# Optimization experiments

Measured on AMD Instinct MI355X. Metric: run time of the kernel, lower is better.

The kernel has to match this reference:

```python
import jax, jax.numpy as jnp
import numpy as np

B, S, H, NH = 8, 1024, 1024, 16
HD = H // NH  # 64


def setup_inputs() -> dict:
    key = jax.random.key(0)
    ks = jax.random.split(key, 7)
    scale = 1.0 / np.sqrt(H)
    return {
        "hidden_states": jax.random.normal(ks[0], (B, S, H), jnp.float32),
        "Wq": jax.random.normal(ks[1], (H, H), jnp.float32) * scale,
        "bq": jax.random.normal(ks[2], (H,), jnp.float32) * 0.01,
        "Wk": jax.random.normal(ks[3], (H, H), jnp.float32) * scale,
        "bk": jax.random.normal(ks[4], (H,), jnp.float32) * 0.01,
        "Wv": jax.random.normal(ks[5], (H, H), jnp.float32) * scale,
        "bv": jax.random.normal(ks[6], (H,), jnp.float32) * 0.01,
    }


def _split_heads(x):
    # [B, S, H] -> [B, NH, S, HD]
    b, s, _ = x.shape
    return x.reshape(b, s, NH, HD).transpose(0, 2, 1, 3)


def reference(hidden_states, Wq, bq, Wk, bk, Wv, bv):
    q = _split_heads(hidden_states @ Wq.T + bq)
    k = _split_heads(hidden_states @ Wk.T + bk)
    v = _split_heads(hidden_states @ Wv.T + bv)
    scale = 1.0 / np.sqrt(HD).astype(np.float32)
    # [B, NH, S, S] attention logits (module materializes this fully)
    scores = jnp.einsum('bhld,bhsd->bhls', q, k) * scale
    probs = jax.nn.softmax(scores, axis=-1)  # dropout_p=0.0 -> no dropout
    ctx = jnp.einsum('bhls,bhsd->bhld', probs, v)
    # [B, NH, S, HD] -> [B, S, H]
    ctx = ctx.transpose(0, 2, 1, 3).reshape(hidden_states.shape[0], hidden_states.shape[1], H)
    return ctx
```

## Files before the change

kernel.cpp:

```cpp
#include <hip/hip_runtime.h>
#include <hip/hip_bf16.h>
#include <stdint.h>

#define B_  8
#define S_  1024
#define H_  1024
#define NH_ 16
#define HD_ 64
#define M_  (B_*S_)

using bf16x8 = __attribute__((ext_vector_type(8))) __bf16;
using f32x4  = __attribute__((ext_vector_type(4))) float;
using f32x16 = __attribute__((ext_vector_type(16))) float;
typedef int iv2 __attribute__((ext_vector_type(2)));

#define LOG2E 1.4426950408889634f

#if __has_builtin(__builtin_amdgcn_exp2f)
#define EXP2(x) __builtin_amdgcn_exp2f(x)
#else
#define EXP2(x) exp2f(x)
#endif

#define SBAR() asm volatile("s_barrier" ::: "memory")
#define WAITV(n) asm volatile("s_waitcnt vmcnt(" #n ")" ::: "memory")

__device__ __forceinline__ void gload_lds16(const void* g, void* l) {
  __builtin_amdgcn_global_load_lds(
      (const __attribute__((address_space(1))) unsigned int*)g,
      (__attribute__((address_space(3))) unsigned int*)l, 16, 0, 0);
}

__device__ __forceinline__ unsigned pack_bf16(float lo, float hi) {
  unsigned r;
  asm("v_cvt_pk_bf16_f32 %0, %1, %2" : "=v"(r) : "v"(lo), "v"(hi));
  return r;
}

__device__ __forceinline__ void swapl32(unsigned& a, unsigned& b) {
#if __has_builtin(__builtin_amdgcn_permlane32_swap)
  iv2 r = __builtin_amdgcn_permlane32_swap((int)a, (int)b, false, false);
  a = (unsigned)r[0];
  b = (unsigned)r[1];
#else
  unsigned axc = (unsigned)__shfl_xor((int)a, 32);
  unsigned bxc = (unsigned)__shfl_xor((int)b, 32);
  int lane = threadIdx.x & 63;
  unsigned an = (lane < 32) ? a : bxc;
  unsigned bn = (lane < 32) ? axc : b;
  a = an; b = bn;
#endif
}

__global__ void __launch_bounds__(256) cast_bf16_kernel(const float* __restrict__ in,
                                                        __bf16* __restrict__ out, int n8) {
  int i = blockIdx.x * blockDim.x + threadIdx.x;
  int stride = gridDim.x * blockDim.x;
  for (; i < n8; i += stride) {
    float4 f0 = ((const float4*)in)[2 * i];
    float4 f1 = ((const float4*)in)[2 * i + 1];
    bf16x8 o;
    o[0] = (__bf16)f0.x; o[1] = (__bf16)f0.y; o[2] = (__bf16)f0.z; o[3] = (__bf16)f0.w;
    o[4] = (__bf16)f1.x; o[5] = (__bf16)f1.y; o[6] = (__bf16)f1.z; o[7] = (__bf16)f1.w;
    ((bf16x8*)out)[i] = o;
  }
}

__global__ void __launch_bounds__(256) cast3_bf16_kernel(
    const float* __restrict__ s0, const float* __restrict__ s1,
    const float* __restrict__ s2, __bf16* __restrict__ dst) {
  int i = blockIdx.x * blockDim.x + threadIdx.x;
  int seg = i >> 17, rem = i & 131071;
  const float* s = (seg == 0) ? s0 : ((seg == 1) ? s1 : s2);
  float4 f0 = ((const float4*)s)[2 * rem];
  float4 f1 = ((const float4*)s)[2 * rem + 1];
  bf16x8 o;
  o[0] = (__bf16)f0.x; o[1] = (__bf16)f0.y; o[2] = (__bf16)f0.z; o[3] = (__bf16)f0.w;
  o[4] = (__bf16)f1.x; o[5] = (__bf16)f1.y; o[6] = (__bf16)f1.z; o[7] = (__bf16)f1.w;
  ((bf16x8*)dst)[i] = o;
}

__global__ void __launch_bounds__(256) qkv_gemm_kernel(
    const __bf16* __restrict__ X,
    const __bf16* __restrict__ Wq, const __bf16* __restrict__ Wk, const __bf16* __restrict__ Wv,
    const float* __restrict__ bq, const float* __restrict__ bk, const float* __restrict__ bv,
    __bf16* __restrict__ Qo, __bf16* __restrict__ Ko, __bf16* __restrict__ Vto) {
  __shared__ __align__(16) char Asm[128 * 128];
  __shared__ __align__(16) char Bsm[128 * 128];

  const int tid = threadIdx.x;
  const int lane = tid & 63, w = tid >> 6;
  const int l15 = lane & 15, g = lane >> 4;
  const int wr = w >> 1, wc = w & 1;
  const int m0 = blockIdx.x * 128;
  const int n0 = blockIdx.y * 128;
  const int z = blockIdx.z;
  const __bf16* W = (z == 0) ? Wq : ((z == 1) ? Wk : Wv);
  const float* bias = (z == 0) ? bq : ((z == 1) ? bk : bv);

  f32x4 acc[4][4] = {};

  for (int kt = 0; kt < H_; kt += 64) {
    __syncthreads();
#pragma unroll
    for (int is = 0; is < 4; ++is) {
      int q = is * 4096 + tid * 16;
      int row = q >> 7;
      int inrow = (q & 127) ^ ((row & 7) << 4);
      const char* ga = (const char*)X + (size_t)(m0 + row) * (H_ * 2) + kt * 2 + inrow;
      const char* gb = (const char*)W + (size_t)(n0 + row) * (H_ * 2) + kt * 2 + inrow;
      gload_lds16(ga, Asm + is * 4096 + w * 1024);
      gload_lds16(gb, Bsm + is * 4096 + w * 1024);
    }
    __syncthreads();
#pragma unroll
    for (int ks = 0; ks < 2; ++ks) {
      bf16x8 a[4], b[4];
#pragma unroll
      for (int i = 0; i < 4; ++i) {
        int row = wr * 64 + i * 16 + l15;
        int chunk = (g + ks * 4) ^ (row & 7);
        a[i] = *reinterpret_cast<const bf16x8*>(Asm + row * 128 + chunk * 16);
      }
#pragma unroll
      for (int j = 0; j < 4; ++j) {
        int row = wc * 64 + j * 16 + l15;
        int chunk = (g + ks * 4) ^ (row & 7);
        b[j] = *reinterpret_cast<const bf16x8*>(Bsm + row * 128 + chunk * 16);
      }
#pragma unroll
      for (int i = 0; i < 4; ++i)
#pragma unroll
        for (int j = 0; j < 4; ++j)
          acc[i][j] = __builtin_amdgcn_mfma_f32_16x16x32_bf16(a[i], b[j], acc[i][j], 0, 0, 0);
    }
  }

#pragma unroll
  for (int i = 0; i < 4; ++i) {
#pragma unroll
    for (int j = 0; j < 4; ++j) {
      int n = n0 + wc * 64 + j * 16 + l15;
      float bs = bias[n];
      int nh = n >> 6, d = n & 63;
#pragma unroll
      for (int r = 0; r < 4; ++r) {
        int m = m0 + wr * 64 + i * 16 + 4 * g + r;
        int bb = m >> 10, s = m & 1023;
        float v = acc[i][j][r] + bs;
        if (z == 0) {
          Qo[(((size_t)bb * NH_ + nh) * S_ + s) * HD_ + d] = (__bf16)(v * (0.125f * LOG2E));
        } else if (z == 1) {
          Ko[(((size_t)bb * NH_ + nh) * S_ + s) * HD_ + d] = (__bf16)v;
        } else {
          Vto[(((size_t)bb * NH_ + nh) * HD_ + d) * S_ + s] = (__bf16)v;
        }
      }
    }
  }
}

#define CROW(r, hi) (((r) & 3) + 8 * ((r) >> 2) + 4 * (hi))

__global__ void __launch_bounds__(512) attn_kernel(
    const __bf16* __restrict__ Q,
    const __bf16* __restrict__ K,
    const __bf16* __restrict__ Vt,
    float* __restrict__ Out) {
  __shared__ __align__(16) char Ksm[2][8192];
  __shared__ __align__(16) char Vsm[2][8192];
  __shared__ __align__(16) float stat_lds[512];

  const int tid = threadIdx.x, lane = tid & 63, w = tid >> 6;
  const int l31 = lane & 31, hi = lane >> 5;
  const int head = blockIdx.y;
  const int bb = head >> 4, nh = head & 15;
  const int qw = blockIdx.x * 256 + w * 32;

  const char* Qh = (const char*)(Q + (size_t)head * S_ * HD_);
  const char* Kh = (const char*)(K + (size_t)head * S_ * HD_);
  const char* Vh = (const char*)(Vt + (size_t)head * S_ * HD_);

  const int srow = (tid * 16) >> 7;
  const int sinrow = ((tid * 16) & 127) ^ ((srow & 7) << 4);

  bf16x8 qf[4];
#pragma unroll
  for (int slot = 0; slot < 4; ++slot)
    qf[slot] = *reinterpret_cast<const bf16x8*>(
        Qh + (size_t)(qw + l31) * 128 + slot * 32 + hi * 16);

  float m_run = -1e30f, l_run = 0.0f;
  f32x16 accO[2] = {};

  gload_lds16(Kh + (size_t)srow * 128 + sinrow, Ksm[0] + w * 1024);
  gload_lds16(Vh + (size_t)srow * 2048 + sinrow, Vsm[0] + w * 1024);

  for (int t = 0; t < 16; ++t) {
    const int cur = t & 1;
    if (t < 15) {
      const int nxt = cur ^ 1;
      const size_t kvn = (size_t)(t + 1) * 64;
      gload_lds16(Kh + (size_t)(kvn + srow) * 128 + sinrow, Ksm[nxt] + w * 1024);
      gload_lds16(Vh + (size_t)srow * 2048 + kvn * 2 + sinrow, Vsm[nxt] + w * 1024);
      WAITV(2);
    } else {
      WAITV(0);
    }
    SBAR();

    const char* Kc = Ksm[cur];
    const char* Vc = Vsm[cur];

    f32x16 s0 = {}, s1 = {};
    __builtin_amdgcn_s_setprio(1);
#pragma unroll
    for (int slot = 0; slot < 4; ++slot) {
      int c0 = slot * 2 + hi;
      int r0 = l31;
      bf16x8 k0 = *reinterpret_cast<const bf16x8*>(Kc + r0 * 128 + ((c0 ^ (r0 & 7)) << 4));
      int r1 = 32 + l31;
      bf16x8 k1 = *reinterpret_cast<const bf16x8*>(Kc + r1 * 128 + ((c0 ^ (r1 & 7)) << 4));
      s0 = __builtin_amdgcn_mfma_f32_32x32x16_bf16(k0, qf[slot], s0, 0, 0, 0);
      s1 = __builtin_amdgcn_mfma_f32_32x32x16_bf16(k1, qf[slot], s1, 0, 0, 0);
    }
    __builtin_amdgcn_s_setprio(0);

    float mx = -1e30f;
#pragma unroll
    for (int r = 0; r < 16; ++r) mx = fmaxf(mx, fmaxf(s0[r], s1[r]));
    mx = fmaxf(mx, __shfl_xor(mx, 32));
    float mnew = fmaxf(m_run, mx);
    float corr = EXP2(m_run - mnew);
    float sum = 0.0f;
#pragma unroll
    for (int r = 0; r < 16; ++r) {
      float p0 = EXP2(s0[r] - mnew); s0[r] = p0; sum += p0;
      float p1 = EXP2(s1[r] - mnew); s1[r] = p1; sum += p1;
    }
    sum += __shfl_xor(sum, 32);
    l_run = l_run * corr + sum;
    m_run = mnew;

    stat_lds[w * 64 + lane] = corr;
    f32x4 c4[4];
#pragma unroll
    for (int rq = 0; rq < 4; ++rq)
      c4[rq] = *reinterpret_cast<const f32x4*>(&stat_lds[w * 64 + rq * 8 + hi * 4]);
#pragma unroll
    for (int r = 0; r < 16; ++r) {
      float cr = c4[r >> 2][r & 3];
      accO[0][r] *= cr;
      accO[1][r] *= cr;
    }

    bf16x8 pa[4];
#define BUILD_PA(T, rb)                                                     \
    {                                                                       \
      unsigned x1 = pack_bf16(T[rb + 0], T[rb + 1]);                        \
      unsigned x2 = pack_bf16(T[rb + 2], T[rb + 3]);                        \
      unsigned y1 = pack_bf16(T[rb + 4], T[rb + 5]);                        \
      unsigned y2 = pack_bf16(T[rb + 6], T[rb + 7]);                        \
      swapl32(x1, y1);                                                      \
      swapl32(x2, y2);                                                      \
      union { unsigned u[4]; bf16x8 v; } cvt;                               \
      cvt.u[0] = x1; cvt.u[1] = x2; cvt.u[2] = y1; cvt.u[3] = y2;           \
      pa_out = cvt.v;                                                       \
    }
    {
      bf16x8 pa_out;
      BUILD_PA(s0, 0) pa[0] = pa_out;
      BUILD_PA(s0, 8) pa[1] = pa_out;
      BUILD_PA(s1, 0) pa[2] = pa_out;
      BUILD_PA(s1, 8) pa[3] = pa_out;
    }

    __builtin_amdgcn_s_setprio(1);
#pragma unroll
    for (int ks = 0; ks < 4; ++ks) {
#pragma unroll
      for (int dt = 0; dt < 2; ++dt) {
        int rd = dt * 32 + l31;
        int ck = ks * 2 + hi;
        bf16x8 vb = *reinterpret_cast<const bf16x8*>(Vc + rd * 128 + ((ck ^ (rd & 7)) << 4));
        accO[dt] = __builtin_amdgcn_mfma_f32_32x32x16_bf16(pa[ks], vb, accO[dt], 0, 0, 0);
      }
    }
    __builtin_amdgcn_s_setprio(0);

    SBAR();
  }

  stat_lds[w * 64 + lane] = 1.0f / l_run;
  f32x4 li4[4];
#pragma unroll
  for (int rq = 0; rq < 4; ++rq)
    li4[rq] = *reinterpret_cast<const f32x4*>(&stat_lds[w * 64 + rq * 8 + hi * 4]);

  float* Ob = Out + (size_t)bb * S_ * H_ + (size_t)nh * HD_;
#pragma unroll
  for (int r = 0; r < 16; ++r) {
    int qabs = qw + CROW(r, hi);
    float li = li4[r >> 2][r & 3];
#pragma unroll
    for (int dt = 0; dt < 2; ++dt) {
      int d = dt * 32 + l31;
      Ob[(size_t)qabs * H_ + d] = accO[dt][r] * li;
    }
  }
}

extern "C" void kernel_launch(void* const* d_in, const int* in_sizes, int n_in,
                              void* d_out, int out_size, void* d_ws, size_t ws_size,
                              hipStream_t stream) {
  const float* hs = (const float*)d_in[0];
  const float* Wq = (const float*)d_in[1];
  const float* bq = (const float*)d_in[2];
  const float* Wk = (const float*)d_in[3];
  const float* bk = (const float*)d_in[4];
  const float* Wv = (const float*)d_in[5];
  const float* bv = (const float*)d_in[6];
  float* out = (float*)d_out;
  char* ws = (char*)d_ws;

  size_t off = 0;
  __bf16* Xb  = (__bf16*)(ws + off); off += (size_t)M_ * H_ * 2;
  __bf16* Wqb = (__bf16*)(ws + off); off += (size_t)H_ * H_ * 2;
  __bf16* Wkb = (__bf16*)(ws + off); off += (size_t)H_ * H_ * 2;
  __bf16* Wvb = (__bf16*)(ws + off); off += (size_t)H_ * H_ * 2;
  __bf16* Qb  = (__bf16*)(ws + off); off += (size_t)M_ * H_ * 2;
  __bf16* Kb  = (__bf16*)(ws + off); off += (size_t)M_ * H_ * 2;
  __bf16* Vtb = (__bf16*)(ws + off); off += (size_t)M_ * H_ * 2;

  cast_bf16_kernel<<<4096, 256, 0, stream>>>(hs, Xb, M_ * H_ / 8);
  cast3_bf16_kernel<<<1536, 256, 0, stream>>>(Wq, Wk, Wv, Wqb);

  qkv_gemm_kernel<<<dim3(M_ / 128, H_ / 128, 3), 256, 0, stream>>>(
      Xb, Wqb, Wkb, Wvb, bq, bk, bv, Qb, Kb, Vtb);

  attn_kernel<<<dim3(S_ / 256, B_ * NH_), 512, 0, stream>>>(Qb, Kb, Vtb, out);
}
```

Before: 150.6 us.

## Rewrite QKV GEMM with 256x192 tiles, double-buffered LDS pipeline, fused weight matrix

The QKV projection GEMM now treats the three weight matrices as one concatenated 3072-wide matrix and uses 512-thread blocks computing 256x192 tiles. K-tile loads go into double-buffered dynamic LDS (112 KB) and are interleaved with the MFMA phases, using s_setprio and partial vmcnt waits. A swizzled block index is added for L2 locality. The goal is to hide global load latency and raise MFMA utilization over the single-buffered 128x128 version, at the cost of heavy LDS use that limits occupancy and a more fragile synchronization scheme.

```diff
diff --git a/kernel.cpp b/kernel.cpp
--- a/kernel.cpp
+++ b/kernel.cpp
@@ -80,80 +80,178 @@
   ((bf16x8*)dst)[i] = o;
 }
 
-__global__ void __launch_bounds__(256) qkv_gemm_kernel(
-    const __bf16* __restrict__ X,
-    const __bf16* __restrict__ Wq, const __bf16* __restrict__ Wk, const __bf16* __restrict__ Wv,
+#define LDSA(s) (lds + (size_t)(s) * 32768)
+#define LDSB(s) (lds + 65536 + (size_t)(s) * 24576)
+
+__global__ void __launch_bounds__(512, 2) qkv_gemm_kernel(
+    const __bf16* __restrict__ X, const __bf16* __restrict__ Wcat,
     const float* __restrict__ bq, const float* __restrict__ bk, const float* __restrict__ bv,
     __bf16* __restrict__ Qo, __bf16* __restrict__ Ko, __bf16* __restrict__ Vto) {
-  __shared__ __align__(16) char Asm[128 * 128];
-  __shared__ __align__(16) char Bsm[128 * 128];
+  extern __shared__ char lds[];
 
   const int tid = threadIdx.x;
   const int lane = tid & 63, w = tid >> 6;
   const int l15 = lane & 15, g = lane >> 4;
-  const int wr = w >> 1, wc = w & 1;
-  const int m0 = blockIdx.x * 128;
-  const int n0 = blockIdx.y * 128;
-  const int z = blockIdx.z;
-  const __bf16* W = (z == 0) ? Wq : ((z == 1) ? Wk : Wv);
-  const float* bias = (z == 0) ? bq : ((z == 1) ? bk : bv);
-
-  f32x4 acc[4][4] = {};
-
-  for (int kt = 0; kt < H_; kt += 64) {
-    __syncthreads();
-#pragma unroll
-    for (int is = 0; is < 4; ++is) {
-      int q = is * 4096 + tid * 16;
-      int row = q >> 7;
-      int inrow = (q & 127) ^ ((row & 7) << 4);
-      const char* ga = (const char*)X + (size_t)(m0 + row) * (H_ * 2) + kt * 2 + inrow;
-      const char* gb = (const char*)W + (size_t)(n0 + row) * (H_ * 2) + kt * 2 + inrow;
-      gload_lds16(ga, Asm + is * 4096 + w * 1024);
-      gload_lds16(gb, Bsm + is * 4096 + w * 1024);
-    }
-    __syncthreads();
-#pragma unroll
-    for (int ks = 0; ks < 2; ++ks) {
-      bf16x8 a[4], b[4];
-#pragma unroll
-      for (int i = 0; i < 4; ++i) {
-        int row = wr * 64 + i * 16 + l15;
-        int chunk = (g + ks * 4) ^ (row & 7);
-        a[i] = *reinterpret_cast<const bf16x8*>(Asm + row * 128 + chunk * 16);
-      }
-#pragma unroll
-      for (int j = 0; j < 4; ++j) {
-        int row = wc * 64 + j * 16 + l15;
-        int chunk = (g + ks * 4) ^ (row & 7);
-        b[j] = *reinterpret_cast<const bf16x8*>(Bsm + row * 128 + chunk * 16);
-      }
-#pragma unroll
-      for (int i = 0; i < 4; ++i)
-#pragma unroll
-        for (int j = 0; j < 4; ++j)
-          acc[i][j] = __builtin_amdgcn_mfma_f32_16x16x32_bf16(a[i], b[j], acc[i][j], 0, 0, 0);
+  const int wm = w >> 2, wn = w & 3;
+
+  const int bid = blockIdx.x;
+  const int swz = ((bid & 7) << 6) | (bid >> 3);
+  const int tm = swz >> 4, tn = swz & 15;
+  const int bm0 = tm * 256, n0 = tn * 192;
+
+  const char* Xb = (const char*)X;
+  const char* Wb = (const char*)Wcat;
+
+  const int row_b = tid >> 3, scB = ((tid & 7) ^ (row_b & 7));
+  const int row_a = tid >> 2, scA = ((tid & 3) ^ ((row_a >> 1) & 3));
+  const char* srcB = Wb + (size_t)(n0 + row_b) * 2048 + scB * 16;
+  const char* srcA = Xb + (size_t)(bm0 + row_a) * 2048 + scA * 16;
+
+#define STG_B(ss, r, ktb) gload_lds16(srcB + (size_t)(r) * 131072 + (ktb), \
+                                      LDSB(ss) + (r) * 8192 + w * 1024)
+#define STG_A(ss, h, rb, ktb) gload_lds16(srcA + (size_t)(rb) * 262144 + (h) * 64 + (ktb), \
+                                          LDSA(ss) + (h) * 16384 + (rb) * 8192 + w * 1024)
+
+  const int aoff = (wm * 128 + l15) * 64 + ((g ^ ((l15 >> 1) & 3)) << 4);
+  const int boffs = (wn * 48 + l15) * 128;
+  const int bsw = l15 & 7;
+
+  f32x4 acc[8][3] = {};
+
+  STG_B(0, 0, 0); STG_B(0, 1, 0); STG_B(0, 2, 0);
+  STG_A(0, 0, 0, 0); STG_A(0, 0, 1, 0);
+  STG_A(0, 1, 0, 0); STG_A(0, 1, 1, 0);
+
+#pragma unroll 2
+  for (int t = 0; t < 16; ++t) {
+    const int s = t & 1, ns = s ^ 1;
+    const bool st = t < 15;
+    const size_t ktb = (size_t)(t + 1) * 128;
+    const char* As = LDSA(s);
+    const char* Bs = LDSB(s);
+
+    WAITV(2);
+    SBAR();
+    bf16x8 b0 = *(const bf16x8*)(Bs + boffs + 0 * 2048 + ((g ^ bsw) << 4));
+    bf16x8 b1 = *(const bf16x8*)(Bs + boffs + 1 * 2048 + ((g ^ bsw) << 4));
+    bf16x8 b2 = *(const bf16x8*)(Bs + boffs + 2 * 2048 + ((g ^ bsw) << 4));
+    {
+      bf16x8 a0 = *(const bf16x8*)(As + aoff + 0 * 1024);
+      bf16x8 a1 = *(const bf16x8*)(As + aoff + 1 * 1024);
+      bf16x8 a2 = *(const bf16x8*)(As + aoff + 2 * 1024);
+      bf16x8 a3 = *(const bf16x8*)(As + aoff + 3 * 1024);
+      if (st) { STG_B(ns, 0, ktb); STG_B(ns, 1, ktb); }
+      __builtin_amdgcn_s_setprio(1);
+      acc[0][0] = __builtin_amdgcn_mfma_f32_16x16x32_bf16(a0, b0, acc[0][0], 0, 0, 0);
+      acc[0][1] = __builtin_amdgcn_mfma_f32_16x16x32_bf16(a0, b1, acc[0][1], 0, 0, 0);
+      acc[0][2] = __builtin_amdgcn_mfma_f32_16x16x32_bf16(a0, b2, acc[0][2], 0, 0, 0);
+      acc[1][0] = __builtin_amdgcn_mfma_f32_16x16x32_bf16(a1, b0, acc[1][0], 0, 0, 0);
+      acc[1][1] = __builtin_amdgcn_mfma_f32_16x16x32_bf16(a1, b1, acc[1][1], 0, 0, 0);
+      acc[1][2] = __builtin_amdgcn_mfma_f32_16x16x32_bf16(a1, b2, acc[1][2], 0, 0, 0);
+      acc[2][0] = __builtin_amdgcn_mfma_f32_16x16x32_bf16(a2, b0, acc[2][0], 0, 0, 0);
+      acc[2][1] = __builtin_amdgcn_mfma_f32_16x16x32_bf16(a2, b1, acc[2][1], 0, 0, 0);
+      acc[2][2] = __builtin_amdgcn_mfma_f32_16x16x32_bf16(a2, b2, acc[2][2], 0, 0, 0);
+      acc[3][0] = __builtin_amdgcn_mfma_f32_16x16x32_bf16(a3, b0, acc[3][0], 0, 0, 0);
+      acc[3][1] = __builtin_amdgcn_mfma_f32_16x16x32_bf16(a3, b1, acc[3][1], 0, 0, 0);
+      acc[3][2] = __builtin_amdgcn_mfma_f32_16x16x32_bf16(a3, b2, acc[3][2], 0, 0, 0);
+      __builtin_amdgcn_s_setprio(0);
+    }
+
+    SBAR();
+    {
+      bf16x8 a4 = *(const bf16x8*)(As + aoff + 4 * 1024);
+      bf16x8 a5 = *(const bf16x8*)(As + aoff + 5 * 1024);
+      bf16x8 a6 = *(const bf16x8*)(As + aoff + 6 * 1024);
+      bf16x8 a7 = *(const bf16x8*)(As + aoff + 7 * 1024);
+      if (st) { STG_B(ns, 2, ktb); STG_A(ns, 0, 0, ktb); }
+      __builtin_amdgcn_s_setprio(1);
+      acc[4][0] = __builtin_amdgcn_mfma_f32_16x16x32_bf16(a4, b0, acc[4][0], 0, 0, 0);
+      acc[4][1] = __builtin_amdgcn_mfma_f32_16x16x32_bf16(a4, b1, acc[4][1], 0, 0, 0);
+      acc[4][2] = __builtin_amdgcn_mfma_f32_16x16x32_bf16(a4, b2, acc[4][2], 0, 0, 0);
+      acc[5][0] = __builtin_amdgcn_mfma_f32_16x16x32_bf16(a5, b0, acc[5][0], 0, 0, 0);
+      acc[5][1] = __builtin_amdgcn_mfma_f32_16x16x32_bf16(a5, b1, acc[5][1], 0, 0, 0);
+      acc[5][2] = __builtin_amdgcn_mfma_f32_16x16x32_bf16(a5, b2, acc[5][2], 0, 0, 0);
+      acc[6][0] = __builtin_amdgcn_mfma_f32_16x16x32_bf16(a6, b0, acc[6][0], 0, 0, 0);
+      acc[6][1] = __builtin_amdgcn_mfma_f32_16x16x32_bf16(a6, b1, acc[6][1], 0, 0, 0);
+      acc[6][2] = __builtin_amdgcn_mfma_f32_16x16x32_bf16(a6, b2, acc[6][2], 0, 0, 0);
+      acc[7][0] = __builtin_amdgcn_mfma_f32_16x16x32_bf16(a7, b0, acc[7][0], 0, 0, 0);
+      acc[7][1] = __builtin_amdgcn_mfma_f32_16x16x32_bf16(a7, b1, acc[7][1], 0, 0, 0);
+      acc[7][2] = __builtin_amdgcn_mfma_f32_16x16x32_bf16(a7, b2, acc[7][2], 0, 0, 0);
+      __builtin_amdgcn_s_setprio(0);
+    }
+
+    if (st) { WAITV(4); } else { WAITV(0); }
+    SBAR();
+    b0 = *(const bf16x8*)(Bs + boffs + 0 * 2048 + (((g + 4) ^ bsw) << 4));
+    b1 = *(const bf16x8*)(Bs + boffs + 1 * 2048 + (((g + 4) ^ bsw) << 4));
+    b2 = *(const bf16x8*)(Bs + boffs + 2 * 2048 + (((g + 4) ^ bsw) << 4));
+    {
+      bf16x8 a0 = *(const bf16x8*)(As + 16384 + aoff + 0 * 1024);
+      bf16x8 a1 = *(const bf16x8*)(As + 16384 + aoff + 1 * 1024);
+      bf16x8 a2 = *(const bf16x8*)(As + 16384 + aoff + 2 * 1024);
+      bf16x8 a3 = *(const bf16x8*)(As + 16384 + aoff + 3 * 1024);
+      if (st) { STG_A(ns, 0, 1, ktb); STG_A(ns, 1, 0, ktb); }
+      __builtin_amdgcn_s_setprio(1);
+      acc[0][0] = __builtin_amdgcn_mfma_f32_16x16x32_bf16(a0, b0, acc[0][0], 0, 0, 0);
+      acc[0][1] = __builtin_amdgcn_mfma_f32_16x16x32_bf16(a0, b1, acc[0][1], 0, 0, 0);
+      acc[0][2] = __builtin_amdgcn_mfma_f32_16x16x32_bf16(a0, b2, acc[0][2], 0, 0, 0);
+      acc[1][0] = __builtin_amdgcn_mfma_f32_16x16x32_bf16(a1, b0, acc[1][0], 0, 0, 0);
+      acc[1][1] = __builtin_amdgcn_mfma_f32_16x16x32_bf16(a1, b1, acc[1][1], 0, 0, 0);
+      acc[1][2] = __builtin_amdgcn_mfma_f32_16x16x32_bf16(a1, b2, acc[1][2], 0, 0, 0);
+      acc[2][0] = __builtin_amdgcn_mfma_f32_16x16x32_bf16(a2, b0, acc[2][0], 0, 0, 0);
+      acc[2][1] = __builtin_amdgcn_mfma_f32_16x16x32_bf16(a2, b1, acc[2][1], 0, 0, 0);
+      acc[2][2] = __builtin_amdgcn_mfma_f32_16x16x32_bf16(a2, b2, acc[2][2], 0, 0, 0);
+      acc[3][0] = __builtin_amdgcn_mfma_f32_16x16x32_bf16(a3, b0, acc[3][0], 0, 0, 0);
+      acc[3][1] = __builtin_amdgcn_mfma_f32_16x16x32_bf16(a3, b1, acc[3][1], 0, 0, 0);
+      acc[3][2] = __builtin_amdgcn_mfma_f32_16x16x32_bf16(a3, b2, acc[3][2], 0, 0, 0);
+      __builtin_amdgcn_s_setprio(0);
+    }
+
+    SBAR();
+    {
+      bf16x8 a4 = *(const bf16x8*)(As + 16384 + aoff + 4 * 1024);
+      bf16x8 a5 = *(const bf16x8*)(As + 16384 + aoff + 5 * 1024);
+      bf16x8 a6 = *(const bf16x8*)(As + 16384 + aoff + 6 * 1024);
+      bf16x8 a7 = *(const bf16x8*)(As + 16384 + aoff + 7 * 1024);
+      if (st) { STG_A(ns, 1, 1, ktb); }
+      __builtin_amdgcn_s_setprio(1);
+      acc[4][0] = __builtin_amdgcn_mfma_f32_16x16x32_bf16(a4, b0, acc[4][0], 0, 0, 0);
+      acc[4][1] = __builtin_amdgcn_mfma_f32_16x16x32_bf16(a4, b1, acc[4][1], 0, 0, 0);
+      acc[4][2] = __builtin_amdgcn_mfma_f32_16x16x32_bf16(a4, b2, acc[4][2], 0, 0, 0);
+      acc[5][0] = __builtin_amdgcn_mfma_f32_16x16x32_bf16(a5, b0, acc[5][0], 0, 0, 0);
+      acc[5][1] = __builtin_amdgcn_mfma_f32_16x16x32_bf16(a5, b1, acc[5][1], 0, 0, 0);
+      acc[5][2] = __builtin_amdgcn_mfma_f32_16x16x32_bf16(a5, b2, acc[5][2], 0, 0, 0);
+      acc[6][0] = __builtin_amdgcn_mfma_f32_16x16x32_bf16(a6, b0, acc[6][0], 0, 0, 0);
+      acc[6][1] = __builtin_amdgcn_mfma_f32_16x16x32_bf16(a6, b1, acc[6][1], 0, 0, 0);
+      acc[6][2] = __builtin_amdgcn_mfma_f32_16x16x32_bf16(a6, b2, acc[6][2], 0, 0, 0);
+      acc[7][0] = __builtin_amdgcn_mfma_f32_16x16x32_bf16(a7, b0, acc[7][0], 0, 0, 0);
+      acc[7][1] = __builtin_amdgcn_mfma_f32_16x16x32_bf16(a7, b1, acc[7][1], 0, 0, 0);
+      acc[7][2] = __builtin_amdgcn_mfma_f32_16x16x32_bf16(a7, b2, acc[7][2], 0, 0, 0);
+      __builtin_amdgcn_s_setprio(0);
     }
   }
 
 #pragma unroll
-  for (int i = 0; i < 4; ++i) {
-#pragma unroll
-    for (int j = 0; j < 4; ++j) {
-      int n = n0 + wc * 64 + j * 16 + l15;
-      float bs = bias[n];
-      int nh = n >> 6, d = n & 63;
+  for (int nf = 0; nf < 3; ++nf) {
+    const int ng = n0 + wn * 48 + nf * 16 + l15;
+    const int z = ng >> 10;
+    const int nzn = ng & 1023;
+    const float* bp = (z == 0) ? bq : ((z == 1) ? bk : bv);
+    const float bs = bp[nzn];
+    const int nh = nzn >> 6, d = nzn & 63;
+#pragma unroll
+    for (int mf = 0; mf < 8; ++mf) {
 #pragma unroll
       for (int r = 0; r < 4; ++r) {
-        int m = m0 + wr * 64 + i * 16 + 4 * g + r;
-        int bb = m >> 10, s = m & 1023;
-        float v = acc[i][j][r] + bs;
+        const int m = bm0 + wm * 128 + mf * 16 + 4 * g + r;
+        const int bb = m >> 10, sI = m & 1023;
+        const float v = acc[mf][nf][r] + bs;
         if (z == 0) {
-          Qo[(((size_t)bb * NH_ + nh) * S_ + s) * HD_ + d] = (__bf16)(v * (0.125f * LOG2E));
+          Qo[(((size_t)bb * NH_ + nh) * S_ + sI) * HD_ + d] = (__bf16)(v * (0.125f * LOG2E));
         } else if (z == 1) {
-          Ko[(((size_t)bb * NH_ + nh) * S_ + s) * HD_ + d] = (__bf16)v;
+          Ko[(((size_t)bb * NH_ + nh) * S_ + sI) * HD_ + d] = (__bf16)v;
         } else {
-          Vto[(((size_t)bb * NH_ + nh) * HD_ + d) * S_ + s] = (__bf16)v;
+          Vto[(((size_t)bb * NH_ + nh) * HD_ + d) * S_ + sI] = (__bf16)v;
         }
       }
     }
@@ -331,12 +429,16 @@
   __bf16* Qb  = (__bf16*)(ws + off); off += (size_t)M_ * H_ * 2;
   __bf16* Kb  = (__bf16*)(ws + off); off += (size_t)M_ * H_ * 2;
   __bf16* Vtb = (__bf16*)(ws + off); off += (size_t)M_ * H_ * 2;
+  (void)Wkb; (void)Wvb;
+
+  (void)hipFuncSetAttribute((const void*)qkv_gemm_kernel,
+                            hipFuncAttributeMaxDynamicSharedMemorySize, 114688);
 
   cast_bf16_kernel<<<4096, 256, 0, stream>>>(hs, Xb, M_ * H_ / 8);
   cast3_bf16_kernel<<<1536, 256, 0, stream>>>(Wq, Wk, Wv, Wqb);
 
-  qkv_gemm_kernel<<<dim3(M_ / 128, H_ / 128, 3), 256, 0, stream>>>(
-      Xb, Wqb, Wkb, Wvb, bq, bk, bv, Qb, Kb, Vtb);
+  qkv_gemm_kernel<<<512, 512, 114688, stream>>>(
+      Xb, Wqb, bq, bk, bv, Qb, Kb, Vtb);
 
   attn_kernel<<<dim3(S_ / 256, B_ * NH_), 512, 0, stream>>>(Qb, Kb, Vtb, out);
 }
```

After: 152.8 us. About the same (+1.4%).

## Double-buffer QKV GEMM LDS tiles with K=32 steps and async prefetch

Applied to the files above, without the earlier changes.

The QKV projection GEMM moves from a single 64-wide K tile with two full barriers per step to double-buffered 32-wide K tiles. The next tile is issued with global-to-LDS loads before the MFMAs on the current tile, and partial vmcnt waits are used. The swizzle is changed to suit 64-byte rows, and MFMA sections get raised wave priority. The aim is to hide global load latency behind compute, at the cost of twice as many loop iterations and barriers.

```diff
diff --git a/kernel.cpp b/kernel.cpp
--- a/kernel.cpp
+++ b/kernel.cpp
@@ -85,8 +85,8 @@
     const __bf16* __restrict__ Wq, const __bf16* __restrict__ Wk, const __bf16* __restrict__ Wv,
     const float* __restrict__ bq, const float* __restrict__ bk, const float* __restrict__ bv,
     __bf16* __restrict__ Qo, __bf16* __restrict__ Ko, __bf16* __restrict__ Vto) {
-  __shared__ __align__(16) char Asm[128 * 128];
-  __shared__ __align__(16) char Bsm[128 * 128];
+  __shared__ __align__(16) char Asm[2][8192];
+  __shared__ __align__(16) char Bsm[2][8192];
 
   const int tid = threadIdx.x;
   const int lane = tid & 63, w = tid >> 6;
@@ -98,42 +98,61 @@
   const __bf16* W = (z == 0) ? Wq : ((z == 1) ? Wk : Wv);
   const float* bias = (z == 0) ? bq : ((z == 1) ? bk : bv);
 
+  const int srow0 = tid >> 2;
+  const int schunk0 = (tid & 3) ^ ((srow0 >> 1) & 3);
+  const int srow1 = 64 + srow0;
+  const int schunk1 = (tid & 3) ^ ((srow1 >> 1) & 3);
+  const char* gA0 = (const char*)X + (size_t)(m0 + srow0) * 2048 + schunk0 * 16;
+  const char* gA1 = (const char*)X + (size_t)(m0 + srow1) * 2048 + schunk1 * 16;
+  const char* gB0 = (const char*)W + (size_t)(n0 + srow0) * 2048 + schunk0 * 16;
+  const char* gB1 = (const char*)W + (size_t)(n0 + srow1) * 2048 + schunk1 * 16;
+
   f32x4 acc[4][4] = {};
 
-  for (int kt = 0; kt < H_; kt += 64) {
-    __syncthreads();
-#pragma unroll
-    for (int is = 0; is < 4; ++is) {
-      int q = is * 4096 + tid * 16;
-      int row = q >> 7;
-      int inrow = (q & 127) ^ ((row & 7) << 4);
-      const char* ga = (const char*)X + (size_t)(m0 + row) * (H_ * 2) + kt * 2 + inrow;
-      const char* gb = (const char*)W + (size_t)(n0 + row) * (H_ * 2) + kt * 2 + inrow;
-      gload_lds16(ga, Asm + is * 4096 + w * 1024);
-      gload_lds16(gb, Bsm + is * 4096 + w * 1024);
-    }
-    __syncthreads();
-#pragma unroll
-    for (int ks = 0; ks < 2; ++ks) {
-      bf16x8 a[4], b[4];
-#pragma unroll
-      for (int i = 0; i < 4; ++i) {
-        int row = wr * 64 + i * 16 + l15;
-        int chunk = (g + ks * 4) ^ (row & 7);
-        a[i] = *reinterpret_cast<const bf16x8*>(Asm + row * 128 + chunk * 16);
-      }
-#pragma unroll
-      for (int j = 0; j < 4; ++j) {
-        int row = wc * 64 + j * 16 + l15;
-        int chunk = (g + ks * 4) ^ (row & 7);
-        b[j] = *reinterpret_cast<const bf16x8*>(Bsm + row * 128 + chunk * 16);
-      }
-#pragma unroll
-      for (int i = 0; i < 4; ++i)
-#pragma unroll
-        for (int j = 0; j < 4; ++j)
-          acc[i][j] = __builtin_amdgcn_mfma_f32_16x16x32_bf16(a[i], b[j], acc[i][j], 0, 0, 0);
-    }
+  gload_lds16(gA0, Asm[0] + w * 1024);
+  gload_lds16(gA1, Asm[0] + 4096 + w * 1024);
+  gload_lds16(gB0, Bsm[0] + w * 1024);
+  gload_lds16(gB1, Bsm[0] + 4096 + w * 1024);
+
+  for (int t = 0; t < 32; ++t) {
+    const int cur = t & 1;
+    if (t < 31) {
+      const int nxt = cur ^ 1;
+      const size_t kb = (size_t)(t + 1) * 64;
+      gload_lds16(gA0 + kb, Asm[nxt] + w * 1024);
+      gload_lds16(gA1 + kb, Asm[nxt] + 4096 + w * 1024);
+      gload_lds16(gB0 + kb, Bsm[nxt] + w * 1024);
+      gload_lds16(gB1 + kb, Bsm[nxt] + 4096 + w * 1024);
+      WAITV(4);
+    } else {
+      WAITV(0);
+    }
+    SBAR();
+
+    const char* As = Asm[cur];
+    const char* Bs = Bsm[cur];
+    bf16x8 a[4], b[4];
+#pragma unroll
+    for (int i = 0; i < 4; ++i) {
+      int row = wr * 64 + i * 16 + l15;
+      int chunk = g ^ ((row >> 1) & 3);
+      a[i] = *reinterpret_cast<const bf16x8*>(As + row * 64 + chunk * 16);
+    }
+#pragma unroll
+    for (int j = 0; j < 4; ++j) {
+      int row = wc * 64 + j * 16 + l15;
+      int chunk = g ^ ((row >> 1) & 3);
+      b[j] = *reinterpret_cast<const bf16x8*>(Bs + row * 64 + chunk * 16);
+    }
+    __builtin_amdgcn_s_setprio(1);
+#pragma unroll
+    for (int i = 0; i < 4; ++i)
+#pragma unroll
+      for (int j = 0; j < 4; ++j)
+        acc[i][j] = __builtin_amdgcn_mfma_f32_16x16x32_bf16(a[i], b[j], acc[i][j], 0, 0, 0);
+    __builtin_amdgcn_s_setprio(0);
+
+    SBAR();
   }
 
 #pragma unroll
```

After: 151.3 us. About the same (+0.4%).
